# Performance work log

Measured on AMD Instinct MI355X. Metric: run time of the kernel, lower is better.

## Reference

```python
import jax, jax.numpy as jnp
import numpy as np

NUM_GROUPS = 32
EPS = 1e-5


def group_norm(x, scale, bias):
    # x: [B, C, H, W]
    B, C, H, W = x.shape
    g = x.reshape(B, NUM_GROUPS, C // NUM_GROUPS * H * W)
    mean = g.mean(axis=-1, keepdims=True)
    var = g.var(axis=-1, keepdims=True)
    g = (g - mean) * jax.lax.rsqrt(var + EPS)
    g = g.reshape(B, C, H, W)
    return g * scale[None, :, None, None] + bias[None, :, None, None]


def conv1x1(x, w, b):
    # x: [B, C, H, W], w: [O, C], b: [O]
    return jnp.einsum('bchw,oc->bohw', x, w) + b[None, :, None, None]


def setup_inputs() -> dict:
    key = jax.random.key(0)
    ks = jax.random.split(key, 11)
    B, C, H, W = 32, 256, 32, 32
    s = 1.0 / np.sqrt(C)
    return {
        'x': jax.random.normal(ks[0], (B, C, H, W), jnp.float32),
        'gn_scale': jnp.ones((C,), jnp.float32),
        'gn_bias': jnp.zeros((C,), jnp.float32),
        'wq': jax.random.normal(ks[1], (C, C), jnp.float32) * s,
        'bq': jnp.zeros((C,), jnp.float32),
        'wk': jax.random.normal(ks[2], (C, C), jnp.float32) * s,
        'bk': jnp.zeros((C,), jnp.float32),
        'wv': jax.random.normal(ks[3], (C, C), jnp.float32) * s,
        'bv': jnp.zeros((C,), jnp.float32),
        'wo': jax.random.normal(ks[4], (C, C), jnp.float32) * s,
        'bo': jnp.zeros((C,), jnp.float32),
    }


def reference(x, gn_scale, gn_bias, wq, bq, wk, bk, wv, bv, wo, bo):
    B, C, H, W = x.shape
    h = group_norm(x, gn_scale, gn_bias)
    q = conv1x1(h, wq, bq).reshape(B, C, H * W)  # [B, C, N]
    k = conv1x1(h, wk, bk).reshape(B, C, H * W)
    v = conv1x1(h, wv, bv).reshape(B, C, H * W)
    # scores: [B, N, N]
    w = jnp.einsum('bcn,bcm->bnm', q, k) * (C ** -0.5)
    w = jax.nn.softmax(w, axis=-1)
    o = jnp.einsum('bnm,bcm->bcn', w, v).reshape(B, C, H, W)
    o = conv1x1(o, wo, bo)
    return x + o
```

## Files before the change

kernel.cpp:

```cpp
#include <hip/hip_runtime.h>

typedef __attribute__((ext_vector_type(4))) float f32x4;
typedef __attribute__((ext_vector_type(8))) short bf16x8;

__device__ __forceinline__ unsigned short f2bf(float f) {
  union { float f; unsigned u; } v; v.f = f;
  unsigned r = (v.u + 0x7FFFu + ((v.u >> 16) & 1u)) >> 16;
  return (unsigned short)r;
}

__device__ __forceinline__ void load16_lds(const void* g, void* l) {
  __builtin_amdgcn_global_load_lds(
      (__attribute__((address_space(1))) void*)(uintptr_t)g,
      (__attribute__((address_space(3))) void*)(unsigned int)(uintptr_t)l,
      16, 0, 0);
}

__global__ __launch_bounds__(256) void convert_w(
    const float* __restrict__ w0, const float* __restrict__ w1,
    const float* __restrict__ w2, const float* __restrict__ w3,
    unsigned short* __restrict__ o0, unsigned short* __restrict__ o1,
    unsigned short* __restrict__ o2, unsigned short* __restrict__ o3) {
  const float* src[4] = {w0, w1, w2, w3};
  unsigned short* dst[4] = {o0, o1, o2, o3};
  int ti = blockIdx.y;
  int idx = blockIdx.x * 256 + threadIdx.x;
  float4 v = ((const float4*)src[ti])[idx];
  ushort4 r;
  r.x = f2bf(v.x); r.y = f2bf(v.y); r.z = f2bf(v.z); r.w = f2bf(v.w);
  ((ushort4*)dst[ti])[idx] = r;
}

__global__ __launch_bounds__(256) void gn_kernel(
    const float* __restrict__ x, const float* __restrict__ gamma,
    const float* __restrict__ beta, unsigned short* __restrict__ h) {
  __shared__ float xs[8 * 1024];
  __shared__ float red[16];
  const int t = threadIdx.x;
  const int b = blockIdx.x >> 5, g = blockIdx.x & 31;
  const float* xp = x + (size_t)(b * 256 + g * 8) * 1024;
  float s = 0.f, ss = 0.f;
#pragma unroll
  for (int j = 0; j < 8; ++j) {
    float4 v = ((const float4*)xp)[j * 256 + t];
    ((float4*)xs)[j * 256 + t] = v;
    s += v.x + v.y + v.z + v.w;
    ss += v.x * v.x + v.y * v.y + v.z * v.z + v.w * v.w;
  }
#pragma unroll
  for (int o = 32; o >= 1; o >>= 1) {
    s += __shfl_xor(s, o);
    ss += __shfl_xor(ss, o);
  }
  const int wave = t >> 6, lane = t & 63;
  if (lane == 0) { red[wave] = s; red[wave + 4] = ss; }
  __syncthreads();
  s = red[0] + red[1] + red[2] + red[3];
  ss = red[4] + red[5] + red[6] + red[7];
  float mean = s * (1.f / 8192.f);
  float var = ss * (1.f / 8192.f) - mean * mean;
  float rstd = rsqrtf(var + 1e-5f);
  float a[8], c[8];
#pragma unroll
  for (int ci = 0; ci < 8; ++ci) {
    float gm = gamma[g * 8 + ci], bt = beta[g * 8 + ci];
    a[ci] = rstd * gm;
    c[ci] = bt - mean * rstd * gm;
  }
  unsigned short* hb = h + (size_t)b * 1024 * 256 + g * 8;
#pragma unroll
  for (int j = 0; j < 4; ++j) {
    int n = j * 256 + t;
    float f0 = xs[0 * 1024 + n] * a[0] + c[0];
    float f1 = xs[1 * 1024 + n] * a[1] + c[1];
    float f2 = xs[2 * 1024 + n] * a[2] + c[2];
    float f3 = xs[3 * 1024 + n] * a[3] + c[3];
    float f4 = xs[4 * 1024 + n] * a[4] + c[4];
    float f5 = xs[5 * 1024 + n] * a[5] + c[5];
    float f6 = xs[6 * 1024 + n] * a[6] + c[6];
    float f7 = xs[7 * 1024 + n] * a[7] + c[7];
    uint4 o4;
    o4.x = (unsigned)f2bf(f0) | ((unsigned)f2bf(f1) << 16);
    o4.y = (unsigned)f2bf(f2) | ((unsigned)f2bf(f3) << 16);
    o4.z = (unsigned)f2bf(f4) | ((unsigned)f2bf(f5) << 16);
    o4.w = (unsigned)f2bf(f6) | ((unsigned)f2bf(f7) << 16);
    *(uint4*)(hb + (size_t)n * 256) = o4;
  }
}

template <bool OUT_F32, int BIAS_MODE, bool HAS_RES>
__global__ __launch_bounds__(256) void gemm_bt(
    const unsigned short* __restrict__ A, long long sAb,
    const unsigned short* __restrict__ Bm, long long sBb,
    void* __restrict__ Cv, long long sCb,
    const float* __restrict__ bias,
    const float* __restrict__ res, long long sRb,
    int M, int N, int K, float alpha) {
  __shared__ unsigned short As[128 * 32];
  __shared__ unsigned short Bs[128 * 32];
  const int t = threadIdx.x;
  const int wave = t >> 6, lane = t & 63;
  const int bm = blockIdx.y * 128, bn = blockIdx.x * 128;
  const int bz = blockIdx.z;
  const unsigned short* Ab = A + (size_t)bz * sAb;
  const unsigned short* Bb = Bm + (size_t)bz * sBb;
  const int wm = (wave >> 1) * 64, wn = (wave & 1) * 64;
  const int srow = t >> 2;
  const int schunk = t & 3;
  const int lrow = lane & 15, kg = lane >> 4;

  f32x4 acc[4][4] = {};

  for (int k0 = 0; k0 < K; k0 += 32) {
#pragma unroll
    for (int r = 0; r < 2; ++r) {
      int row = r * 64 + srow;
      int cs = schunk ^ ((row >> 1) & 3);
      const unsigned short* ga = Ab + (size_t)(bm + row) * K + (k0 + cs * 8);
      const unsigned short* gb = Bb + (size_t)(bn + row) * K + (k0 + cs * 8);
      load16_lds(ga, &As[(r * 64 + wave * 16) * 32]);
      load16_lds(gb, &Bs[(r * 64 + wave * 16) * 32]);
    }
    __syncthreads();
    bf16x8 af[4], bfr[4];
#pragma unroll
    for (int i = 0; i < 4; ++i) {
      int ra = wm + i * 16 + lrow;
      af[i] = *(const bf16x8*)&As[ra * 32 + ((kg ^ ((ra >> 1) & 3)) * 8)];
      int rb = wn + i * 16 + lrow;
      bfr[i] = *(const bf16x8*)&Bs[rb * 32 + ((kg ^ ((rb >> 1) & 3)) * 8)];
    }
#pragma unroll
    for (int i = 0; i < 4; ++i)
#pragma unroll
      for (int j = 0; j < 4; ++j)
        acc[i][j] = __builtin_amdgcn_mfma_f32_16x16x32_bf16(af[i], bfr[j], acc[i][j], 0, 0, 0);
    __syncthreads();
  }

#pragma unroll
  for (int i = 0; i < 4; ++i) {
#pragma unroll
    for (int j = 0; j < 4; ++j) {
#pragma unroll
      for (int r = 0; r < 4; ++r) {
        int m = bm + wm + i * 16 + (lane >> 4) * 4 + r;
        int n = bn + wn + j * 16 + lrow;
        float v = acc[i][j][r] * alpha;
        if constexpr (BIAS_MODE == 1) v += bias[m];
        if constexpr (BIAS_MODE == 2) v += bias[n];
        if constexpr (HAS_RES) v += res[(size_t)bz * sRb + (size_t)m * N + n];
        if constexpr (OUT_F32)
          ((float*)Cv)[(size_t)bz * sCb + (size_t)m * N + n] = v;
        else
          ((unsigned short*)Cv)[(size_t)bz * sCb + (size_t)m * N + n] = f2bf(v);
      }
    }
  }
}

__global__ __launch_bounds__(512, 1) void flash_attn(
    const unsigned short* __restrict__ qt,
    const unsigned short* __restrict__ kt,
    const unsigned short* __restrict__ vt,
    unsigned short* __restrict__ ot) {
  __shared__ unsigned short Ks[2][64 * 256];
  __shared__ unsigned short Vs[2][256 * 64];
  __shared__ unsigned short Pl[128 * 72];
  __shared__ float red[2 * 128];

  const int t = threadIdx.x;
  const int wave = t >> 6, lane = t & 63;
  const int wr = wave >> 1, wc = wave & 1;
  const int lrow = lane & 15, hi = lane >> 4;

  const int lbid = blockIdx.x;
  const int logical = (lbid & 7) * 32 + (lbid >> 3);
  const int b = logical >> 3;
  const int q0 = (logical & 7) * 128;

  const unsigned short* qb = qt + (size_t)b * 1024 * 256;
  const unsigned short* kb = kt + (size_t)b * 1024 * 256;
  const unsigned short* vb = vt + (size_t)b * 1024 * 256;

#pragma unroll
  for (int p = 0; p < 4; ++p) {
    int row = p * 16 + wave * 2 + (lane >> 5);
    int ch = (lane & 31) ^ (row & 31);
    load16_lds(kb + (size_t)row * 256 + ch * 8, &Ks[0][(p * 16 + wave * 2) * 256]);
  }
#pragma unroll
  for (int p = 0; p < 4; ++p) {
    int row = p * 64 + wave * 8 + (lane >> 3);
    int ch = (lane & 7) ^ (row & 7);
    load16_lds(vb + (size_t)row * 1024 + ch * 8, &Vs[0][(p * 64 + wave * 8) * 64]);
  }

  bf16x8 aq[2][8];
#pragma unroll
  for (int i = 0; i < 2; ++i)
#pragma unroll
    for (int kk = 0; kk < 8; ++kk)
      aq[i][kk] = *(const bf16x8*)(qb + (size_t)(q0 + wr * 32 + i * 16 + lrow) * 256 + kk * 32 + hi * 8);

  f32x4 acco[2][8] = {};
  float lsumP[2][4] = {{0.f, 0.f, 0.f, 0.f}, {0.f, 0.f, 0.f, 0.f}};

  asm volatile("s_waitcnt vmcnt(0)" ::: "memory");
  __builtin_amdgcn_s_barrier();
  __builtin_amdgcn_sched_barrier(0);

  const float SC2 = 0.0625f * 1.44269504f;

  for (int tt = 0; tt < 16; ++tt) {
    const int cur = tt & 1, nxt = cur ^ 1;

    if (tt < 15) {
      const int m0n = (tt + 1) * 64;
#pragma unroll
      for (int p = 0; p < 4; ++p) {
        int row = p * 16 + wave * 2 + (lane >> 5);
        int ch = (lane & 31) ^ (row & 31);
        load16_lds(kb + (size_t)(m0n + row) * 256 + ch * 8, &Ks[nxt][(p * 16 + wave * 2) * 256]);
      }
#pragma unroll
      for (int p = 0; p < 4; ++p) {
        int row = p * 64 + wave * 8 + (lane >> 3);
        int ch = (lane & 7) ^ (row & 7);
        load16_lds(vb + (size_t)row * 1024 + m0n + ch * 8, &Vs[nxt][(p * 64 + wave * 8) * 64]);
      }
    }

    f32x4 accs[2][2] = {};
    __builtin_amdgcn_s_setprio(1);
#pragma unroll
    for (int kk = 0; kk < 8; ++kk) {
#pragma unroll
      for (int j = 0; j < 2; ++j) {
        int m = wc * 32 + j * 16 + lrow;
        bf16x8 bk8 = *(const bf16x8*)&Ks[cur][m * 256 + (((kk * 4 + hi) ^ (m & 31)) * 8)];
        accs[0][j] = __builtin_amdgcn_mfma_f32_16x16x32_bf16(aq[0][kk], bk8, accs[0][j], 0, 0, 0);
        accs[1][j] = __builtin_amdgcn_mfma_f32_16x16x32_bf16(aq[1][kk], bk8, accs[1][j], 0, 0, 0);
      }
    }
    __builtin_amdgcn_s_setprio(0);

#pragma unroll
    for (int i = 0; i < 2; ++i)
#pragma unroll
      for (int j = 0; j < 2; ++j)
#pragma unroll
        for (int r = 0; r < 4; ++r) {
          float e = exp2f(accs[i][j][r] * SC2);
          lsumP[i][r] += e;
          Pl[(wr * 32 + i * 16 + hi * 4 + r) * 72 + wc * 32 + j * 16 + lrow] = f2bf(e);
        }

    asm volatile("s_waitcnt lgkmcnt(0)" ::: "memory");
    __builtin_amdgcn_s_barrier();
    __builtin_amdgcn_sched_barrier(0);

#pragma unroll
    for (int kk2 = 0; kk2 < 2; ++kk2) {
      bf16x8 pa0 = *(const bf16x8*)&Pl[(wr * 32 + 0 * 16 + lrow) * 72 + kk2 * 32 + hi * 8];
      bf16x8 pa1 = *(const bf16x8*)&Pl[(wr * 32 + 1 * 16 + lrow) * 72 + kk2 * 32 + hi * 8];
      __builtin_amdgcn_s_setprio(1);
#pragma unroll
      for (int jj = 0; jj < 8; ++jj) {
        int c = wc * 128 + jj * 16 + lrow;
        bf16x8 bv8 = *(const bf16x8*)&Vs[cur][c * 64 + (((kk2 * 4 + hi) ^ (c & 7)) * 8)];
        acco[0][jj] = __builtin_amdgcn_mfma_f32_16x16x32_bf16(pa0, bv8, acco[0][jj], 0, 0, 0);
        acco[1][jj] = __builtin_amdgcn_mfma_f32_16x16x32_bf16(pa1, bv8, acco[1][jj], 0, 0, 0);
      }
      __builtin_amdgcn_s_setprio(0);
    }

    asm volatile("s_waitcnt vmcnt(0) lgkmcnt(0)" ::: "memory");
    __builtin_amdgcn_s_barrier();
    __builtin_amdgcn_sched_barrier(0);
  }

#pragma unroll
  for (int off = 1; off <= 8; off <<= 1)
#pragma unroll
    for (int i = 0; i < 2; ++i)
#pragma unroll
      for (int r = 0; r < 4; ++r)
        lsumP[i][r] += __shfl_xor(lsumP[i][r], off);
  if (lrow == 0) {
#pragma unroll
    for (int i = 0; i < 2; ++i)
#pragma unroll
      for (int r = 0; r < 4; ++r)
        red[wc * 128 + wr * 32 + i * 16 + hi * 4 + r] = lsumP[i][r];
  }
  __syncthreads();

  unsigned short* ob = ot + (size_t)b * 1024 * 256;
#pragma unroll
  for (int i = 0; i < 2; ++i) {
    float inv[4];
#pragma unroll
    for (int r = 0; r < 4; ++r) {
      int rl = wr * 32 + i * 16 + hi * 4 + r;
      inv[r] = 1.f / (red[rl] + red[128 + rl]);
    }
#pragma unroll
    for (int jj = 0; jj < 8; ++jj)
#pragma unroll
      for (int r = 0; r < 4; ++r) {
        int n = q0 + wr * 32 + i * 16 + hi * 4 + r;
        int c = wc * 128 + jj * 16 + lrow;
        ob[(size_t)n * 256 + c] = f2bf(acco[i][jj][r] * inv[r]);
      }
  }
}

extern "C" void kernel_launch(void* const* d_in, const int* in_sizes, int n_in,
                              void* d_out, int out_size, void* d_ws, size_t ws_size,
                              hipStream_t stream) {
  const float* x    = (const float*)d_in[0];
  const float* gnsc = (const float*)d_in[1];
  const float* gnb  = (const float*)d_in[2];
  const float* wq   = (const float*)d_in[3];
  const float* bq   = (const float*)d_in[4];
  const float* wk   = (const float*)d_in[5];
  const float* bk   = (const float*)d_in[6];
  const float* wv   = (const float*)d_in[7];
  const float* bv   = (const float*)d_in[8];
  const float* wo   = (const float*)d_in[9];
  const float* bo   = (const float*)d_in[10];
  float* out = (float*)d_out;

  unsigned short* wqb = (unsigned short*)d_ws;
  unsigned short* wkb = wqb + 65536;
  unsigned short* wvb = wkb + 65536;
  unsigned short* wob = wvb + 65536;
  unsigned short* h   = wob + 65536;
  unsigned short* qt  = h + 8388608;
  unsigned short* kt  = qt + 8388608;
  unsigned short* vt  = kt + 8388608;
  unsigned short* ot  = h;

  const long long sHN = 1024LL * 256;

  convert_w<<<dim3(64, 4), 256, 0, stream>>>(wq, wk, wv, wo, wqb, wkb, wvb, wob);
  gn_kernel<<<dim3(1024), 256, 0, stream>>>(x, gnsc, gnb, h);
  gemm_bt<false, 2, false><<<dim3(2, 8, 32), 256, 0, stream>>>(
      h, sHN, wqb, 0, qt, sHN, bq, nullptr, 0, 1024, 256, 256, 1.f);
  gemm_bt<false, 2, false><<<dim3(2, 8, 32), 256, 0, stream>>>(
      h, sHN, wkb, 0, kt, sHN, bk, nullptr, 0, 1024, 256, 256, 1.f);
  gemm_bt<false, 1, false><<<dim3(8, 2, 32), 256, 0, stream>>>(
      wvb, 0, h, sHN, vt, sHN, bv, nullptr, 0, 256, 1024, 256, 1.f);
  flash_attn<<<dim3(256), 512, 0, stream>>>(qt, kt, vt, ot);
  gemm_bt<true, 1, true><<<dim3(8, 2, 32), 256, 0, stream>>>(
      wob, 0, ot, sHN, out, sHN, bo, x, sHN, 256, 1024, 256, 1.f);
}
```

Measured before the change: 127.5 us.

## Fuse Q/K projections and software-pipeline PV against next QK in attention

```diff
diff --git a/kernel.cpp b/kernel.cpp
--- a/kernel.cpp
+++ b/kernel.cpp
@@ -7,6 +7,12 @@
   union { float f; unsigned u; } v; v.f = f;
   unsigned r = (v.u + 0x7FFFu + ((v.u >> 16) & 1u)) >> 16;
   return (unsigned short)r;
+}
+
+__device__ __forceinline__ unsigned cvt_pk_bf16(float lo, float hi) {
+  unsigned r;
+  asm("v_cvt_pk_bf16_f32 %0, %1, %2" : "=v"(r) : "v"(lo), "v"(hi));
+  return r;
 }
 
 __device__ __forceinline__ void load16_lds(const void* g, void* l) {
@@ -17,18 +23,23 @@
 }
 
 __global__ __launch_bounds__(256) void convert_w(
-    const float* __restrict__ w0, const float* __restrict__ w1,
-    const float* __restrict__ w2, const float* __restrict__ w3,
-    unsigned short* __restrict__ o0, unsigned short* __restrict__ o1,
-    unsigned short* __restrict__ o2, unsigned short* __restrict__ o3) {
-  const float* src[4] = {w0, w1, w2, w3};
-  unsigned short* dst[4] = {o0, o1, o2, o3};
+    const float* __restrict__ wq, const float* __restrict__ wk,
+    const float* __restrict__ wv, const float* __restrict__ wo,
+    const float* __restrict__ bq, const float* __restrict__ bk,
+    unsigned short* __restrict__ wqkb, unsigned short* __restrict__ wvb,
+    unsigned short* __restrict__ wob, float* __restrict__ bqkf) {
+  const float* src[4] = {wq, wk, wv, wo};
+  unsigned short* dst[4] = {wqkb, wqkb + 65536, wvb, wob};
   int ti = blockIdx.y;
   int idx = blockIdx.x * 256 + threadIdx.x;
   float4 v = ((const float4*)src[ti])[idx];
   ushort4 r;
   r.x = f2bf(v.x); r.y = f2bf(v.y); r.z = f2bf(v.z); r.w = f2bf(v.w);
   ((ushort4*)dst[ti])[idx] = r;
+  if (ti == 3 && blockIdx.x == 0) {
+    bqkf[threadIdx.x] = bq[threadIdx.x];
+    bqkf[256 + threadIdx.x] = bk[threadIdx.x];
+  }
 }
 
 __global__ __launch_bounds__(256) void gn_kernel(
@@ -159,15 +170,12 @@
   }
 }
 
-__global__ __launch_bounds__(512, 1) void flash_attn(
-    const unsigned short* __restrict__ qt,
-    const unsigned short* __restrict__ kt,
+__global__ __launch_bounds__(512, 2) void flash_attn(
+    const unsigned short* __restrict__ qk,
     const unsigned short* __restrict__ vt,
     unsigned short* __restrict__ ot) {
-  __shared__ unsigned short Ks[2][64 * 256];
-  __shared__ unsigned short Vs[2][256 * 64];
-  __shared__ unsigned short Pl[128 * 72];
-  __shared__ float red[2 * 128];
+  __shared__ unsigned short SMEM[81920];
+  const int VS = 32768, PB = 65536;
 
   const int t = threadIdx.x;
   const int wave = t >> 6, lane = t & 63;
@@ -179,21 +187,15 @@
   const int b = logical >> 3;
   const int q0 = (logical & 7) * 128;
 
-  const unsigned short* qb = qt + (size_t)b * 1024 * 256;
-  const unsigned short* kb = kt + (size_t)b * 1024 * 256;
+  const unsigned short* qb = qk + (size_t)b * 1024 * 512;
+  const unsigned short* kb = qb + 256;
   const unsigned short* vb = vt + (size_t)b * 1024 * 256;
 
 #pragma unroll
   for (int p = 0; p < 4; ++p) {
     int row = p * 16 + wave * 2 + (lane >> 5);
     int ch = (lane & 31) ^ (row & 31);
-    load16_lds(kb + (size_t)row * 256 + ch * 8, &Ks[0][(p * 16 + wave * 2) * 256]);
-  }
-#pragma unroll
-  for (int p = 0; p < 4; ++p) {
-    int row = p * 64 + wave * 8 + (lane >> 3);
-    int ch = (lane & 7) ^ (row & 7);
-    load16_lds(vb + (size_t)row * 1024 + ch * 8, &Vs[0][(p * 64 + wave * 8) * 64]);
+    load16_lds(kb + (size_t)row * 512 + ch * 8, &SMEM[(p * 16 + wave * 2) * 256]);
   }
 
   bf16x8 aq[2][8];
@@ -201,7 +203,7 @@
   for (int i = 0; i < 2; ++i)
 #pragma unroll
     for (int kk = 0; kk < 8; ++kk)
-      aq[i][kk] = *(const bf16x8*)(qb + (size_t)(q0 + wr * 32 + i * 16 + lrow) * 256 + kk * 32 + hi * 8);
+      aq[i][kk] = *(const bf16x8*)(qb + (size_t)(q0 + wr * 32 + i * 16 + lrow) * 512 + kk * 32 + hi * 8);
 
   f32x4 acco[2][8] = {};
   float lsumP[2][4] = {{0.f, 0.f, 0.f, 0.f}, {0.f, 0.f, 0.f, 0.f}};
@@ -212,67 +214,88 @@
 
   const float SC2 = 0.0625f * 1.44269504f;
 
-  for (int tt = 0; tt < 16; ++tt) {
+  for (int tt = 0; tt <= 16; ++tt) {
     const int cur = tt & 1, nxt = cur ^ 1;
 
     if (tt < 15) {
-      const int m0n = (tt + 1) * 64;
+      const unsigned short* kn = kb + (size_t)(tt + 1) * 64 * 512;
 #pragma unroll
       for (int p = 0; p < 4; ++p) {
         int row = p * 16 + wave * 2 + (lane >> 5);
         int ch = (lane & 31) ^ (row & 31);
-        load16_lds(kb + (size_t)(m0n + row) * 256 + ch * 8, &Ks[nxt][(p * 16 + wave * 2) * 256]);
-      }
+        load16_lds(kn + (size_t)row * 512 + ch * 8, &SMEM[nxt * 16384 + (p * 16 + wave * 2) * 256]);
+      }
+    }
+    if (tt < 16) {
+      const unsigned short* vn = vb + tt * 64;
 #pragma unroll
       for (int p = 0; p < 4; ++p) {
         int row = p * 64 + wave * 8 + (lane >> 3);
         int ch = (lane & 7) ^ (row & 7);
-        load16_lds(vb + (size_t)row * 1024 + m0n + ch * 8, &Vs[nxt][(p * 64 + wave * 8) * 64]);
+        load16_lds(vn + (size_t)row * 1024 + ch * 8, &SMEM[VS + cur * 16384 + (p * 64 + wave * 8) * 64]);
       }
     }
 
     f32x4 accs[2][2] = {};
-    __builtin_amdgcn_s_setprio(1);
-#pragma unroll
-    for (int kk = 0; kk < 8; ++kk) {
-#pragma unroll
-      for (int j = 0; j < 2; ++j) {
-        int m = wc * 32 + j * 16 + lrow;
-        bf16x8 bk8 = *(const bf16x8*)&Ks[cur][m * 256 + (((kk * 4 + hi) ^ (m & 31)) * 8)];
-        accs[0][j] = __builtin_amdgcn_mfma_f32_16x16x32_bf16(aq[0][kk], bk8, accs[0][j], 0, 0, 0);
-        accs[1][j] = __builtin_amdgcn_mfma_f32_16x16x32_bf16(aq[1][kk], bk8, accs[1][j], 0, 0, 0);
-      }
-    }
-    __builtin_amdgcn_s_setprio(0);
-
-#pragma unroll
-    for (int i = 0; i < 2; ++i)
-#pragma unroll
-      for (int j = 0; j < 2; ++j)
-#pragma unroll
-        for (int r = 0; r < 4; ++r) {
-          float e = exp2f(accs[i][j][r] * SC2);
-          lsumP[i][r] += e;
-          Pl[(wr * 32 + i * 16 + hi * 4 + r) * 72 + wc * 32 + j * 16 + lrow] = f2bf(e);
+    if (tt < 16) {
+      const unsigned short* Kp = &SMEM[cur * 16384];
+      __builtin_amdgcn_s_setprio(1);
+#pragma unroll
+      for (int kk = 0; kk < 8; ++kk) {
+#pragma unroll
+        for (int j = 0; j < 2; ++j) {
+          int m = wc * 32 + j * 16 + lrow;
+          bf16x8 bk8 = *(const bf16x8*)&Kp[m * 256 + (((kk * 4 + hi) ^ (m & 31)) * 8)];
+          accs[0][j] = __builtin_amdgcn_mfma_f32_16x16x32_bf16(aq[0][kk], bk8, accs[0][j], 0, 0, 0);
+          accs[1][j] = __builtin_amdgcn_mfma_f32_16x16x32_bf16(aq[1][kk], bk8, accs[1][j], 0, 0, 0);
         }
-
-    asm volatile("s_waitcnt lgkmcnt(0)" ::: "memory");
-    __builtin_amdgcn_s_barrier();
-    __builtin_amdgcn_sched_barrier(0);
-
-#pragma unroll
-    for (int kk2 = 0; kk2 < 2; ++kk2) {
-      bf16x8 pa0 = *(const bf16x8*)&Pl[(wr * 32 + 0 * 16 + lrow) * 72 + kk2 * 32 + hi * 8];
-      bf16x8 pa1 = *(const bf16x8*)&Pl[(wr * 32 + 1 * 16 + lrow) * 72 + kk2 * 32 + hi * 8];
-      __builtin_amdgcn_s_setprio(1);
-#pragma unroll
-      for (int jj = 0; jj < 8; ++jj) {
-        int c = wc * 128 + jj * 16 + lrow;
-        bf16x8 bv8 = *(const bf16x8*)&Vs[cur][c * 64 + (((kk2 * 4 + hi) ^ (c & 7)) * 8)];
-        acco[0][jj] = __builtin_amdgcn_mfma_f32_16x16x32_bf16(pa0, bv8, acco[0][jj], 0, 0, 0);
-        acco[1][jj] = __builtin_amdgcn_mfma_f32_16x16x32_bf16(pa1, bv8, acco[1][jj], 0, 0, 0);
       }
       __builtin_amdgcn_s_setprio(0);
+    }
+
+    if (tt >= 1) {
+      const unsigned short* Pp = &SMEM[PB + nxt * 8192];
+      const unsigned short* Vp = &SMEM[VS + nxt * 16384];
+#pragma unroll
+      for (int kk2 = 0; kk2 < 2; ++kk2) {
+        int qa0 = wr * 32 + lrow;
+        int qa1 = qa0 + 16;
+        bf16x8 pa0 = *(const bf16x8*)&Pp[qa0 * 64 + ((kk2 * 32 + hi * 8) ^ ((qa0 & 7) << 3))];
+        bf16x8 pa1 = *(const bf16x8*)&Pp[qa1 * 64 + ((kk2 * 32 + hi * 8) ^ ((qa1 & 7) << 3))];
+        __builtin_amdgcn_s_setprio(1);
+#pragma unroll
+        for (int jj = 0; jj < 8; ++jj) {
+          int c = wc * 128 + jj * 16 + lrow;
+          bf16x8 bv8 = *(const bf16x8*)&Vp[c * 64 + (((kk2 * 4 + hi) ^ (c & 7)) * 8)];
+          acco[0][jj] = __builtin_amdgcn_mfma_f32_16x16x32_bf16(pa0, bv8, acco[0][jj], 0, 0, 0);
+          acco[1][jj] = __builtin_amdgcn_mfma_f32_16x16x32_bf16(pa1, bv8, acco[1][jj], 0, 0, 0);
+        }
+        __builtin_amdgcn_s_setprio(0);
+      }
+    }
+
+    if (tt < 16) {
+      unsigned short* Pw = &SMEM[PB + cur * 8192];
+#pragma unroll
+      for (int i = 0; i < 2; ++i) {
+        int qb4 = wr * 32 + i * 16 + hi * 4;
+#pragma unroll
+        for (int j = 0; j < 2; ++j) {
+          int kvs = wc * 32 + j * 16 + lrow;
+          float e0 = exp2f(accs[i][j][0] * SC2);
+          float e1 = exp2f(accs[i][j][1] * SC2);
+          float e2 = exp2f(accs[i][j][2] * SC2);
+          float e3 = exp2f(accs[i][j][3] * SC2);
+          lsumP[i][0] += e0; lsumP[i][1] += e1;
+          lsumP[i][2] += e2; lsumP[i][3] += e3;
+          unsigned p01 = cvt_pk_bf16(e0, e1);
+          unsigned p23 = cvt_pk_bf16(e2, e3);
+          Pw[(qb4 + 0) * 64 + (kvs ^ (((qb4 + 0) & 7) << 3))] = (unsigned short)p01;
+          Pw[(qb4 + 1) * 64 + (kvs ^ (((qb4 + 1) & 7) << 3))] = (unsigned short)(p01 >> 16);
+          Pw[(qb4 + 2) * 64 + (kvs ^ (((qb4 + 2) & 7) << 3))] = (unsigned short)p23;
+          Pw[(qb4 + 3) * 64 + (kvs ^ (((qb4 + 3) & 7) << 3))] = (unsigned short)(p23 >> 16);
+        }
+      }
     }
 
     asm volatile("s_waitcnt vmcnt(0) lgkmcnt(0)" ::: "memory");
@@ -287,6 +310,7 @@
 #pragma unroll
       for (int r = 0; r < 4; ++r)
         lsumP[i][r] += __shfl_xor(lsumP[i][r], off);
+  float* red = (float*)SMEM;
   if (lrow == 0) {
 #pragma unroll
     for (int i = 0; i < 2; ++i)
@@ -332,27 +356,25 @@
   const float* bo   = (const float*)d_in[10];
   float* out = (float*)d_out;
 
-  unsigned short* wqb = (unsigned short*)d_ws;
-  unsigned short* wkb = wqb + 65536;
-  unsigned short* wvb = wkb + 65536;
-  unsigned short* wob = wvb + 65536;
-  unsigned short* h   = wob + 65536;
-  unsigned short* qt  = h + 8388608;
-  unsigned short* kt  = qt + 8388608;
-  unsigned short* vt  = kt + 8388608;
-  unsigned short* ot  = h;
+  unsigned short* wqkb = (unsigned short*)d_ws;
+  unsigned short* wvb  = wqkb + 131072;
+  unsigned short* wob  = wvb + 65536;
+  float*          bqkf = (float*)(wob + 65536);
+  unsigned short* h    = wob + 65536 + 2048;
+  unsigned short* qkb  = h + 8388608;
+  unsigned short* vt   = qkb + 16777216;
+  unsigned short* ot   = h;
 
   const long long sHN = 1024LL * 256;
-
-  convert_w<<<dim3(64, 4), 256, 0, stream>>>(wq, wk, wv, wo, wqb, wkb, wvb, wob);
+  const long long sQK = 1024LL * 512;
+
+  convert_w<<<dim3(64, 4), 256, 0, stream>>>(wq, wk, wv, wo, bq, bk, wqkb, wvb, wob, bqkf);
   gn_kernel<<<dim3(1024), 256, 0, stream>>>(x, gnsc, gnb, h);
-  gemm_bt<false, 2, false><<<dim3(2, 8, 32), 256, 0, stream>>>(
-      h, sHN, wqb, 0, qt, sHN, bq, nullptr, 0, 1024, 256, 256, 1.f);
-  gemm_bt<false, 2, false><<<dim3(2, 8, 32), 256, 0, stream>>>(
-      h, sHN, wkb, 0, kt, sHN, bk, nullptr, 0, 1024, 256, 256, 1.f);
+  gemm_bt<false, 2, false><<<dim3(4, 8, 32), 256, 0, stream>>>(
+      h, sHN, wqkb, 0, qkb, sQK, bqkf, nullptr, 0, 1024, 512, 256, 1.f);
   gemm_bt<false, 1, false><<<dim3(8, 2, 32), 256, 0, stream>>>(
       wvb, 0, h, sHN, vt, sHN, bv, nullptr, 0, 256, 1024, 256, 1.f);
-  flash_attn<<<dim3(256), 512, 0, stream>>>(qt, kt, vt, ot);
+  flash_attn<<<dim3(256), 512, 0, stream>>>(qkb, vt, ot);
   gemm_bt<true, 1, true><<<dim3(8, 2, 32), 256, 0, stream>>>(
       wob, 0, ot, sHN, out, sHN, bo, x, sHN, 256, 1024, 256, 1.f);
 }
```

New measurement: 123.7 us. 1.03x faster.
